# Performance work log

Hardware: AMD Instinct MI355X
Metric: run time of the kernel (lower is better)

Reference implementation:

```python
import jax, jax.numpy as jnp
import numpy as np
from jax import lax

B, C, H, W = 4, 512, 64, 64
C8 = C // 8
OUT = 256
BN_EPS = 1e-5


def setup_inputs() -> dict:
    key = jax.random.key(0)
    ks = jax.random.split(key, 12)
    s = lambda k, shape, fan: jax.random.normal(k, shape, jnp.float32) * (1.0 / np.sqrt(fan))
    return {
        "x": jax.random.normal(ks[0], (B, C, H, W), jnp.float32),
        "wq": s(ks[1], (C8, C), C), "bq": jnp.zeros((C8,), jnp.float32),
        "wk": s(ks[2], (C8, C), C), "bk": jnp.zeros((C8,), jnp.float32),
        "wv": s(ks[3], (C, C), C),  "bv": jnp.zeros((C,), jnp.float32),
        "ca_w1": s(ks[4], (C8, C), C),
        "ca_w2": s(ks[5], (C, C8), C8),
        "conv_w": s(ks[6], (OUT, C, 3, 3), C * 9),
        "bn_gamma": jnp.ones((OUT,), jnp.float32),
        "bn_beta": jnp.zeros((OUT,), jnp.float32),
        "bn_mean": jnp.zeros((OUT,), jnp.float32),
        "bn_var": jnp.ones((OUT,), jnp.float32),
    }


def reference(x, wq, bq, wk, bk, wv, bv, ca_w1, ca_w2, conv_w,
              bn_gamma, bn_beta, bn_mean, bn_var):
    b, c, h, w = x.shape
    n = h * w
    xf = x.reshape(b, c, n)  # [B,C,N]

    # ---- Position attention ----
    q = jnp.einsum('qc,bcn->bnq', wq, xf) + bq            # [B,N,C8]
    k = jnp.einsum('kc,bcn->bkn', wk, xf) + bk[:, None]   # [B,C8,N]
    energy = jnp.einsum('bnq,bqm->bnm', q, k)             # [B,N,N]
    attn = jax.nn.softmax(energy, axis=-1)
    v = jnp.einsum('vc,bcn->bvn', wv, xf) + bv[:, None]   # [B,C,N]
    # torch: bmm(value, attention^T) -> out[b,c,m] = sum_n v[b,c,n]*attn[b,m,n]
    pa = jnp.einsum('bcn,bmn->bcm', v, attn).reshape(b, c, h, w) + x

    # ---- Channel attention (SE-style, avg+max pooled, shared MLP) ----
    avg = jnp.mean(pa, axis=(2, 3))   # [B,C]
    mx = jnp.max(pa, axis=(2, 3))     # [B,C]
    fc = lambda z: jnp.einsum('oc,bc->bo', ca_w2,
                              jax.nn.relu(jnp.einsum('hc,bc->bh', ca_w1, z)))
    scale = jax.nn.sigmoid(fc(avg) + fc(mx))[:, :, None, None]
    ca = scale * pa

    # ---- Conv 3x3 + BN (eval mode) + ReLU ----
    y = lax.conv_general_dilated(ca, conv_w, (1, 1), 'SAME',
                                 dimension_numbers=('NCHW', 'OIHW', 'NCHW'))
    inv = lax.rsqrt(bn_var + BN_EPS)
    y = (y - bn_mean[:, None, None]) * (inv * bn_gamma)[:, None, None] + bn_beta[:, None, None]
    return jax.nn.relu(y)
```

## Files before the change

### kernel.cpp

```cpp
#include <hip/hip_runtime.h>

#define NB 4
#define CIN 512
#define NPIX 4096
#define CQK 64
#define COUT 256
#define PPIX 4356

typedef __bf16 bh16;
typedef _Float16 fh16;
typedef __attribute__((ext_vector_type(8))) __bf16 bf16x8;
typedef __attribute__((ext_vector_type(8))) _Float16 f16x8;
typedef __attribute__((ext_vector_type(16))) float f32x16;

#define AS1 __attribute__((address_space(1)))
#define AS3 __attribute__((address_space(3)))

__device__ __forceinline__ void glds16(const void* g, void* l) {
  __builtin_amdgcn_global_load_lds((const AS1 unsigned int*)g, (AS3 unsigned int*)l, 16, 0, 0);
}

__device__ __forceinline__ float fexp2(float x) {
#if __has_builtin(__builtin_amdgcn_exp2f)
  return __builtin_amdgcn_exp2f(x);
#else
  return __expf(x * 0.6931471805599453f);
#endif
}

__global__ __launch_bounds__(256) void transpose_bf_k(const float* __restrict__ src,
                                                      bh16* __restrict__ dst,
                                                      int rows, int cols) {
  __shared__ float tile[32][33];
  const int b = blockIdx.z;
  const int c0 = blockIdx.x * 32;
  const int r0 = blockIdx.y * 32;
  const float* s = src + (size_t)b * rows * cols;
  bh16* d = dst + (size_t)b * rows * cols;
  const int tx = threadIdx.x, ty = threadIdx.y;
#pragma unroll
  for (int i = 0; i < 32; i += 8)
    tile[ty + i][tx] = s[(size_t)(r0 + ty + i) * cols + (c0 + tx)];
  __syncthreads();
#pragma unroll
  for (int i = 0; i < 32; i += 8)
    d[(size_t)(c0 + ty + i) * rows + (r0 + tx)] = (bh16)tile[tx][ty + i];
}

__global__ __launch_bounds__(256) void wcast_k(const float* __restrict__ wq,
                                               const float* __restrict__ wk,
                                               const float* __restrict__ wv,
                                               const float* __restrict__ bq,
                                               const float* __restrict__ bk,
                                               bh16* __restrict__ Wqk,
                                               bh16* __restrict__ wvb,
                                               float* __restrict__ bias128) {
  const int idx = blockIdx.x * 256 + threadIdx.x;
  if (idx < 65536) {
    Wqk[idx] = (bh16)(idx < 32768 ? wq[idx] : wk[idx - 32768]);
  } else {
    const int j = idx - 65536;
    wvb[j] = (bh16)wv[j];
  }
  if (idx < 128) bias128[idx] = idx < 64 ? bq[idx] : bk[idx - 64];
}

__global__ __launch_bounds__(256) void qk_proj_k(const bh16* __restrict__ xTb,
                                                 const bh16* __restrict__ Wqk,
                                                 const float* __restrict__ bias128,
                                                 bh16* __restrict__ Qb,
                                                 bh16* __restrict__ Kf) {
  const int blk = blockIdx.x;
  const int t = threadIdx.x;
  const int w = t >> 6, l31 = t & 31, hi = (t & 63) >> 5;
  __shared__ __align__(16) bh16 As[2][64 * 64];
  f32x16 acc[2];
#pragma unroll
  for (int nt = 0; nt < 2; nt++)
#pragma unroll
    for (int r = 0; r < 16; r++) acc[nt][r] = 0.0f;

#define QK_STAGE(kc, buf)                                                           \
  {                                                                                 \
    _Pragma("unroll") for (int i = 0; i < 2; i++) {                                 \
      const int s = i * 256 + t;                                                    \
      const int n = s >> 3, slot = s & 7;                                           \
      glds16(xTb + (size_t)(blk * 64 + n) * CIN + (kc) * 64 + (((slot + n) & 7) * 8), \
             &As[buf][(size_t)(i * 256 + w * 64) * 8]);                             \
    }                                                                               \
  }

  QK_STAGE(0, 0);
  __syncthreads();
  for (int kc = 0; kc < 8; kc++) {
    if (kc < 7) QK_STAGE(kc + 1, (kc + 1) & 1);
    const bh16* as = As[kc & 1];
#pragma unroll
    for (int ks = 0; ks < 4; ks++) {
      const bf16x8 bfr = *(const bf16x8*)(Wqk + (size_t)(w * 32 + l31) * CIN + kc * 64 + ks * 16 + hi * 8);
      const int kk = ks * 2 + hi;
#pragma unroll
      for (int nt = 0; nt < 2; nt++) {
        const int n = nt * 32 + l31;
        const bf16x8 a = *(const bf16x8*)&as[(size_t)(n * 8 + ((kk - n) & 7)) * 8];
        acc[nt] = __builtin_amdgcn_mfma_f32_32x32x16_bf16(a, bfr, acc[nt], 0, 0, 0);
      }
    }
    __syncthreads();
  }
#undef QK_STAGE
  const int o = w * 32 + l31;
  const float bo = bias128[o];
  if (w < 2) {
#pragma unroll
    for (int nt = 0; nt < 2; nt++)
#pragma unroll
      for (int r = 0; r < 16; r++) {
        const int nloc = nt * 32 + (r & 3) + 8 * (r >> 2) + 4 * hi;
        Qb[(size_t)(blk * 64 + nloc) * 64 + o] = (bh16)((acc[nt][r] + bo) * 1.44269504088896f);
      }
  } else {
    const int b = blk >> 6, jtile = blk & 63;
    const int k = o - 64, kg = k >> 3, k7 = k & 7;
    bh16* kdst = Kf + (((size_t)(b * 64 + jtile) * 8 + kg) * 64) * 8 + k7;
#pragma unroll
    for (int nt = 0; nt < 2; nt++)
#pragma unroll
      for (int r = 0; r < 16; r++) {
        const int j = nt * 32 + (r & 3) + 8 * (r >> 2) + 4 * hi;
        kdst[(size_t)j * 8] = (bh16)(acc[nt][r] + bo);
      }
  }
}

__global__ __launch_bounds__(256) void v_proj_k(const bh16* __restrict__ xTb,
                                                const bh16* __restrict__ wvb,
                                                const float* __restrict__ bv,
                                                bh16* __restrict__ Vf) {
  const int nblk = blockIdx.x;
  const int cblk = blockIdx.y;
  const int b = blockIdx.z;
  const int t = threadIdx.x;
  const int w = t >> 6, l31 = t & 31, hi = (t & 63) >> 5;
  __shared__ __align__(16) bh16 Bs[2][256 * 64];
  f32x16 acc[2][2];
#pragma unroll
  for (int mt = 0; mt < 2; mt++)
#pragma unroll
    for (int nt = 0; nt < 2; nt++)
#pragma unroll
      for (int r = 0; r < 16; r++) acc[mt][nt][r] = 0.0f;

#define V_STAGE(kc, buf)                                                              \
  {                                                                                   \
    _Pragma("unroll") for (int i = 0; i < 8; i++) {                                   \
      const int s = i * 256 + t;                                                      \
      const int n = s >> 3, slot = s & 7;                                             \
      glds16(xTb + (size_t)(b * NPIX + nblk * 256 + n) * CIN + (kc) * 64 + (((slot + n) & 7) * 8), \
             &Bs[buf][(size_t)(i * 256 + w * 64) * 8]);                               \
    }                                                                                 \
  }

  V_STAGE(0, 0);
  __syncthreads();
  for (int kc = 0; kc < 8; kc++) {
    if (kc < 7) V_STAGE(kc + 1, (kc + 1) & 1);
    const bh16* bs = Bs[kc & 1];
#pragma unroll
    for (int ks = 0; ks < 4; ks++) {
      const int kk = ks * 2 + hi;
      bf16x8 a[2], bfr[2];
#pragma unroll
      for (int mt = 0; mt < 2; mt++)
        a[mt] = *(const bf16x8*)(wvb + (size_t)(cblk * 64 + mt * 32 + l31) * CIN + kc * 64 + ks * 16 + hi * 8);
#pragma unroll
      for (int nt = 0; nt < 2; nt++) {
        const int n = w * 64 + nt * 32 + l31;
        bfr[nt] = *(const bf16x8*)&bs[(size_t)(n * 8 + ((kk - n) & 7)) * 8];
      }
#pragma unroll
      for (int mt = 0; mt < 2; mt++)
#pragma unroll
        for (int nt = 0; nt < 2; nt++)
          acc[mt][nt] = __builtin_amdgcn_mfma_f32_32x32x16_bf16(a[mt], bfr[nt], acc[mt][nt], 0, 0, 0);
    }
    __syncthreads();
  }
#undef V_STAGE
  const int ntile0 = nblk * 4 + w;
#pragma unroll
  for (int mt = 0; mt < 2; mt++)
#pragma unroll
    for (int r = 0; r < 16; r++) {
      const int c = cblk * 64 + mt * 32 + (r & 3) + 8 * (r >> 2) + 4 * hi;
      const float bvc = bv[c];
#pragma unroll
      for (int nt = 0; nt < 2; nt++) {
        const int nl = nt * 32 + l31;
        Vf[(((size_t)(b * 64 + ntile0) * 8 + (nl >> 3)) * 512 + c) * 8 + (nl & 7)] =
            (bh16)(acc[mt][nt][r] + bvc);
      }
    }
}

__global__ __launch_bounds__(256, 2) void attn1p_k(const bh16* __restrict__ Qb,
                                                   const bh16* __restrict__ Kf,
                                                   const bh16* __restrict__ Vf,
                                                   const float* __restrict__ x,
                                                   fh16* __restrict__ pa,
                                                   float* __restrict__ psum,
                                                   float* __restrict__ pmax) {
  const int id = blockIdx.x + 2 * (blockIdx.y + 64 * blockIdx.z);
  const int b = (id & 7) >> 1;
  const int cblk = id & 1;
  const int mblk = (id >> 3) * 64;
  const int t = threadIdx.x;
  const int w = t >> 6, l31 = t & 31, hi = (t >> 5) & 1;
  const int jhalf = w & 1, mhalf = w >> 1;
  __shared__ __align__(16) bh16 Ps[2][8 * 64 * 8];
  __shared__ float lred[4][32];
  __shared__ float linvL[64];

  bf16x8 qf[4];
  {
    const bh16* qrow = Qb + (size_t)(b * NPIX + mblk + mhalf * 32 + l31) * 64;
#pragma unroll
    for (int ks = 0; ks < 4; ks++) qf[ks] = *(const bf16x8*)(qrow + ks * 16 + hi * 8);
  }
  const bh16* kfb = Kf + (size_t)b * (64 * 8 * 64 * 8);
  const bh16* vfb = Vf + (size_t)b * (64 * 8 * 512 * 8);
  const int cbase = cblk * 256 + w * 64;

#define KADDR(tile, ks) (kfb + (((size_t)(tile) * 8 + (ks) * 2 + hi) * 64 + jhalf * 32 + l31) * 8)
#define VADDR(tile, ks, ct) (vfb + (((size_t)(tile) * 8 + (ks) * 2 + hi) * 512 + cbase + (ct) * 32 + l31) * 8)

  f32x16 acc[2][2];
#pragma unroll
  for (int mt = 0; mt < 2; mt++)
#pragma unroll
    for (int ct = 0; ct < 2; ct++)
#pragma unroll
      for (int r = 0; r < 16; r++) acc[mt][ct][r] = 0.0f;
  float4 lsacc;
  lsacc.x = 0.0f; lsacc.y = 0.0f; lsacc.z = 0.0f; lsacc.w = 0.0f;

  bf16x8 kf_nxt[4];
  bf16x8 vf_use[4][2];
  f32x16 s1;
  {
    bf16x8 k0[4];
#pragma unroll
    for (int ks = 0; ks < 4; ks++) {
      k0[ks] = *(const bf16x8*)KADDR(0, ks);
#pragma unroll
      for (int ct = 0; ct < 2; ct++) vf_use[ks][ct] = *(const bf16x8*)VADDR(0, ks, ct);
    }
#pragma unroll
    for (int ks = 0; ks < 4; ks++) kf_nxt[ks] = *(const bf16x8*)KADDR(1, ks);
#pragma unroll
    for (int r = 0; r < 16; r++) s1[r] = 0.0f;
#pragma unroll
    for (int ks = 0; ks < 4; ks++)
      s1 = __builtin_amdgcn_mfma_f32_32x32x16_bf16(k0[ks], qf[ks], s1, 0, 0, 0);
  }

  for (int it = 0; it < 64; it++) {
    f32x16 s1n;
#pragma unroll
    for (int r = 0; r < 16; r++) s1n[r] = 0.0f;
#pragma unroll
    for (int ks = 0; ks < 4; ks++)
      s1n = __builtin_amdgcn_mfma_f32_32x32x16_bf16(kf_nxt[ks], qf[ks], s1n, 0, 0, 0);
    {
      const int kt = (it + 2 < 64) ? it + 2 : 63;
#pragma unroll
      for (int ks = 0; ks < 4; ks++) kf_nxt[ks] = *(const bf16x8*)KADDR(kt, ks);
    }

    const bh16* ps = Ps[(it + 1) & 1];
    bh16* psw = Ps[it & 1];
    if (it) {
#pragma unroll
      for (int ks = 0; ks < 4; ks++) {
        bf16x8 pf0 = *(const bf16x8*)&ps[(size_t)((ks * 2 + hi) * 64 + l31) * 8];
        bf16x8 pf1 = *(const bf16x8*)&ps[(size_t)((ks * 2 + hi) * 64 + 32 + l31) * 8];
        acc[0][0] = __builtin_amdgcn_mfma_f32_32x32x16_bf16(pf0, vf_use[ks][0], acc[0][0], 0, 0, 0);
        acc[0][1] = __builtin_amdgcn_mfma_f32_32x32x16_bf16(pf0, vf_use[ks][1], acc[0][1], 0, 0, 0);
        {
          union { bh16 h[4]; uint2 u2; } pk;
#pragma unroll
          for (int q = 0; q < 4; q++) {
            const float p = fexp2(s1[ks * 4 + q]);
            lsacc[q] += p;
            pk.h[q] = (bh16)p;
          }
          *(uint2*)(void*)&psw[(size_t)((jhalf * 4 + ks) * 64 + mhalf * 32 + l31) * 8 + hi * 4] = pk.u2;
        }
        acc[1][0] = __builtin_amdgcn_mfma_f32_32x32x16_bf16(pf1, vf_use[ks][0], acc[1][0], 0, 0, 0);
        acc[1][1] = __builtin_amdgcn_mfma_f32_32x32x16_bf16(pf1, vf_use[ks][1], acc[1][1], 0, 0, 0);
        vf_use[ks][0] = *(const bf16x8*)VADDR(it, ks, 0);
        vf_use[ks][1] = *(const bf16x8*)VADDR(it, ks, 1);
      }
    } else {
#pragma unroll
      for (int g = 0; g < 4; g++) {
        union { bh16 h[4]; uint2 u2; } pk;
#pragma unroll
        for (int q = 0; q < 4; q++) {
          const float p = fexp2(s1[g * 4 + q]);
          lsacc[q] += p;
          pk.h[q] = (bh16)p;
        }
        *(uint2*)(void*)&psw[(size_t)((jhalf * 4 + g) * 64 + mhalf * 32 + l31) * 8 + hi * 4] = pk.u2;
      }
    }
    __syncthreads();
    s1 = s1n;
  }
  {
    const bh16* ps = Ps[1];
#pragma unroll
    for (int ks = 0; ks < 4; ks++) {
      bf16x8 pf0 = *(const bf16x8*)&ps[(size_t)((ks * 2 + hi) * 64 + l31) * 8];
      bf16x8 pf1 = *(const bf16x8*)&ps[(size_t)((ks * 2 + hi) * 64 + 32 + l31) * 8];
      acc[0][0] = __builtin_amdgcn_mfma_f32_32x32x16_bf16(pf0, vf_use[ks][0], acc[0][0], 0, 0, 0);
      acc[0][1] = __builtin_amdgcn_mfma_f32_32x32x16_bf16(pf0, vf_use[ks][1], acc[0][1], 0, 0, 0);
      acc[1][0] = __builtin_amdgcn_mfma_f32_32x32x16_bf16(pf1, vf_use[ks][0], acc[1][0], 0, 0, 0);
      acc[1][1] = __builtin_amdgcn_mfma_f32_32x32x16_bf16(pf1, vf_use[ks][1], acc[1][1], 0, 0, 0);
    }
  }
#undef KADDR
#undef VADDR

  float lsum = (lsacc.x + lsacc.y) + (lsacc.z + lsacc.w);
  lsum += __shfl_xor(lsum, 32);
  if (hi == 0) lred[w][l31] = lsum;
  __syncthreads();
  if (t < 64) linvL[t] = 1.0f / (lred[(t >> 5) * 2][t & 31] + lred[(t >> 5) * 2 + 1][t & 31]);
  __syncthreads();

  float csum[2] = {0.0f, 0.0f};
  float cmax[2] = {-1e30f, -1e30f};
#pragma unroll
  for (int mt = 0; mt < 2; mt++) {
#pragma unroll
    for (int g = 0; g < 4; g++) {
      const int mloc = mt * 32 + g * 8 + hi * 4;
      const float4 lv = *(const float4*)&linvL[mloc];
#pragma unroll
      for (int ct = 0; ct < 2; ct++) {
        const int c = cbase + ct * 32 + l31;
        const float4 xv = *(const float4*)&x[(size_t)(b * CIN + c) * NPIX + mblk + mloc];
        float r0 = acc[mt][ct][g * 4 + 0] * lv.x + xv.x;
        float r1 = acc[mt][ct][g * 4 + 1] * lv.y + xv.y;
        float r2 = acc[mt][ct][g * 4 + 2] * lv.z + xv.z;
        float r3 = acc[mt][ct][g * 4 + 3] * lv.w + xv.w;
        csum[ct] += (r0 + r1) + (r2 + r3);
        cmax[ct] = fmaxf(cmax[ct], fmaxf(fmaxf(r0, r1), fmaxf(r2, r3)));
        fh16* pd = pa + ((size_t)(b * NPIX) + mblk + mloc) * CIN + c;
        pd[0 * CIN] = (fh16)r0;
        pd[1 * CIN] = (fh16)r1;
        pd[2 * CIN] = (fh16)r2;
        pd[3 * CIN] = (fh16)r3;
      }
    }
  }
#pragma unroll
  for (int ct = 0; ct < 2; ct++) {
    csum[ct] += __shfl_xor(csum[ct], 32);
    cmax[ct] = fmaxf(cmax[ct], __shfl_xor(cmax[ct], 32));
  }
  if (hi == 0) {
    const int mb = mblk >> 6;
#pragma unroll
    for (int ct = 0; ct < 2; ct++) {
      const int c = cbase + ct * 32 + l31;
      psum[((size_t)b * 64 + mb) * CIN + c] = csum[ct];
      pmax[((size_t)b * 64 + mb) * CIN + c] = cmax[ct];
    }
  }
}

__global__ __launch_bounds__(256) void mlp2_k(const float* __restrict__ psum,
                                              const float* __restrict__ pmax,
                                              const float* __restrict__ w1,
                                              const float* __restrict__ w2,
                                              float* __restrict__ scale) {
  const int b = blockIdx.x;
  const int t = threadIdx.x;
  __shared__ float avg_l[CIN], max_l[CIN], hbuf[128];
#pragma unroll
  for (int h = 0; h < 2; h++) {
    const int c = t + h * 256;
    float s = 0.0f, m = -1e30f;
#pragma unroll
    for (int k = 0; k < 64; k++) {
      s += psum[((size_t)b * 64 + k) * CIN + c];
      m = fmaxf(m, pmax[((size_t)b * 64 + k) * CIN + c]);
    }
    avg_l[c] = s * (1.0f / 4096.0f);
    max_l[c] = m;
  }
  __syncthreads();
  if (t < 128) {
    const float* src = (t < 64) ? avg_l : max_l;
    const int o = t & 63;
    float sacc = 0.0f;
    for (int c = 0; c < CIN; c++) sacc += w1[o * CIN + c] * src[c];
    hbuf[t] = fmaxf(sacc, 0.0f);
  }
  __syncthreads();
#pragma unroll
  for (int h = 0; h < 2; h++) {
    const int c = t + h * 256;
    float sacc = 0.0f;
#pragma unroll
    for (int k = 0; k < 64; k++) sacc += w2[c * 64 + k] * (hbuf[k] + hbuf[64 + k]);
    scale[b * CIN + c] = 1.0f / (1.0f + __expf(-sacc));
  }
}

__global__ __launch_bounds__(256) void pack_k(const fh16* __restrict__ pa,
                                              const float* __restrict__ scl,
                                              fh16* __restrict__ pab) {
  const int b = blockIdx.y;
  const int n0 = blockIdx.x * 8;
  const int t = threadIdx.x;
  __shared__ float sc[CIN];
#pragma unroll
  for (int h = 0; h < 2; h++) sc[t + h * 256] = scl[b * CIN + t + h * 256];
  __syncthreads();
  const int c2 = t * 2;
  const float s0 = sc[c2], s1 = sc[c2 + 1];
#pragma unroll
  for (int j = 0; j < 8; j++) {
    const int n = n0 + j;
    const int pp = ((n >> 6) + 1) * 66 + (n & 63) + 1;
    union { fh16 h[2]; unsigned int u; } v, o;
    v.u = *(const unsigned int*)(pa + ((size_t)b * NPIX + n) * CIN + c2);
    o.h[0] = (fh16)((float)v.h[0] * s0);
    o.h[1] = (fh16)((float)v.h[1] * s1);
    *(unsigned int*)(void*)(pab + ((size_t)b * PPIX + pp) * CIN + c2) = o.u;
  }
}

__global__ __launch_bounds__(256) void bzero_k(fh16* __restrict__ pab) {
  const int t = threadIdx.x;
  const int p = blockIdx.x * 4 + (t >> 6);
  const int b = blockIdx.y;
  int pp;
  if (p < 66) pp = p;
  else if (p < 132) pp = 65 * 66 + (p - 66);
  else if (p < 196) pp = (p - 131) * 66;
  else pp = (p - 195) * 66 + 65;
  uint4 z = {0u, 0u, 0u, 0u};
  *(uint4*)(void*)(pab + ((size_t)b * PPIX + pp) * CIN + (t & 63) * 8) = z;
}

__global__ __launch_bounds__(256) void wpack_k(const float* __restrict__ cw,
                                               fh16* __restrict__ wp) {
  const int slot = blockIdx.x * 256 + threadIdx.x;
  const int oblk = slot / 36864;
  const int r1 = slot - oblk * 36864;
  const int chunk = r1 / 1152;
  const int r2 = r1 - chunk * 1152;
  const int tap = r2 >> 7;
  const int r3 = r2 & 127;
  const int h = r3 >> 6;
  const int o = r3 & 63;
  const size_t sbase = (size_t)(oblk * 64 + o) * 4608 + (size_t)(chunk * 16 + h * 8) * 9 + tap;
  union { fh16 h8[8]; uint4 u4; } pk;
#pragma unroll
  for (int i = 0; i < 8; i++) pk.h8[i] = (fh16)cw[sbase + (size_t)i * 9];
  *(uint4*)(void*)(wp + (size_t)slot * 8) = pk.u4;
}

__global__ __launch_bounds__(256) void conv_mfma_k(const fh16* __restrict__ pab,
                                                   const fh16* __restrict__ wp,
                                                   const float* __restrict__ gamma,
                                                   const float* __restrict__ beta,
                                                   const float* __restrict__ mean,
                                                   const float* __restrict__ var,
                                                   float* __restrict__ out) {
  const int y0 = blockIdx.x * 4;
  const int oblk = blockIdx.y;
  const int b = blockIdx.z;
  const int t = threadIdx.x;
  const int w = t >> 6, lane = t & 63, l31 = lane & 31, hi = lane >> 5;
  __shared__ __align__(16) fh16 Xs[2][416 * 16];
  __shared__ __align__(16) fh16 Ws[2][9 * 64 * 16];
  __shared__ float sb[64], bb[64];
  if (t < 64) {
    const int o = oblk * 64 + t;
    const float inv = rsqrtf(var[o] + 1e-5f);
    const float sc = inv * gamma[o];
    sb[t] = sc;
    bb[t] = beta[o] - mean[o] * sc;
  }
  f32x16 o00, o01, o10, o11;
#pragma unroll
  for (int r = 0; r < 16; r++) { o00[r] = 0.0f; o01[r] = 0.0f; o10[r] = 0.0f; o11[r] = 0.0f; }

  const fh16* xbase = pab + ((size_t)b * PPIX + y0 * 66) * CIN + (size_t)(lane & 31) * CIN + (lane >> 5) * 8;
  const fh16* wbase = wp + (size_t)oblk * 32 * 9216 + lane * 8;

#define STAGE(chunk, buf)                                                        \
  {                                                                              \
    const fh16* xs = xbase + (chunk) * 16;                                       \
    for (int i = w; i < 13; i += 4)                                              \
      glds16(xs + (size_t)i * 32 * CIN, &Xs[buf][i * 512]);                      \
    const fh16* wsrc = wbase + (size_t)(chunk) * 9216;                           \
    for (int i = w; i < 18; i += 4)                                              \
      glds16(wsrc + (size_t)i * 512, &Ws[buf][i * 512]);                         \
  }

  STAGE(0, 0);
  __syncthreads();
  for (int chunk = 0; chunk < 32; chunk++) {
    if (chunk < 31) STAGE(chunk + 1, (chunk + 1) & 1);
    const fh16* xs = Xs[chunk & 1];
    const fh16* ws = Ws[chunk & 1];
#pragma unroll
    for (int tap = 0; tap < 9; tap++) {
      const int ky = tap / 3, kx = tap - ky * 3;
      const f16x8 a0 = *(const f16x8*)&ws[tap * 1024 + hi * 512 + l31 * 8];
      const f16x8 a1 = *(const f16x8*)&ws[tap * 1024 + hi * 512 + (32 + l31) * 8];
      const int row0 = (w + ky) * 66 + l31 + kx;
      const int row1 = row0 + 32;
      const f16x8 b0 = *(const f16x8*)&xs[(row0 >> 5) * 512 + hi * 256 + (row0 & 31) * 8];
      const f16x8 b1 = *(const f16x8*)&xs[(row1 >> 5) * 512 + hi * 256 + (row1 & 31) * 8];
      o00 = __builtin_amdgcn_mfma_f32_32x32x16_f16(a0, b0, o00, 0, 0, 0);
      o01 = __builtin_amdgcn_mfma_f32_32x32x16_f16(a0, b1, o01, 0, 0, 0);
      o10 = __builtin_amdgcn_mfma_f32_32x32x16_f16(a1, b0, o10, 0, 0, 0);
      o11 = __builtin_amdgcn_mfma_f32_32x32x16_f16(a1, b1, o11, 0, 0, 0);
    }
    __syncthreads();
  }
#undef STAGE

  const f32x16* accs[2][2] = {{&o00, &o01}, {&o10, &o11}};
#pragma unroll
  for (int mt = 0; mt < 2; mt++) {
#pragma unroll
    for (int nt = 0; nt < 2; nt++) {
      const f32x16& A = *accs[mt][nt];
#pragma unroll
      for (int r = 0; r < 16; r++) {
        const int cl = mt * 32 + (r & 3) + 8 * (r >> 2) + 4 * hi;
        const int pix = nt * 32 + l31;
        const float y = A[r] * sb[cl] + bb[cl];
        out[((size_t)(b * COUT + oblk * 64 + cl)) * NPIX + (y0 + w) * 64 + pix] = fmaxf(y, 0.0f);
      }
    }
  }
}

extern "C" void kernel_launch(void* const* d_in, const int* in_sizes, int n_in,
                              void* d_out, int out_size, void* d_ws, size_t ws_size,
                              hipStream_t stream) {
  (void)in_sizes; (void)n_in; (void)out_size; (void)ws_size;
  const float* x        = (const float*)d_in[0];
  const float* wq       = (const float*)d_in[1];
  const float* bq       = (const float*)d_in[2];
  const float* wk       = (const float*)d_in[3];
  const float* bk       = (const float*)d_in[4];
  const float* wv       = (const float*)d_in[5];
  const float* bv       = (const float*)d_in[6];
  const float* ca_w1    = (const float*)d_in[7];
  const float* ca_w2    = (const float*)d_in[8];
  const float* conv_w   = (const float*)d_in[9];
  const float* bn_gamma = (const float*)d_in[10];
  const float* bn_beta  = (const float*)d_in[11];
  const float* bn_mean  = (const float*)d_in[12];
  const float* bn_var   = (const float*)d_in[13];
  float* out = (float*)d_out;

  float* ws = (float*)d_ws;
  fh16*  pa      = (fh16*)ws;
  float* psum    = ws + 4194304;
  float* pmax    = ws + 4325376;
  bh16*  Vf      = (bh16*)(ws + 8388608);
  fh16*  wpck    = (fh16*)(ws + 8388608);
  bh16*  Qb      = (bh16*)(ws + 12582912);
  bh16*  Kf      = (bh16*)(ws + 13107200);
  bh16*  xTb     = (bh16*)(ws + 13631488);
  fh16*  pab     = (fh16*)(ws + 13631488);
  bh16*  Wqk     = (bh16*)(ws + 17825792);
  bh16*  wvb     = (bh16*)(ws + 17858560);
  float* bias128 = ws + 17989632;
  float* scl     = ws + 18104320;

  wcast_k<<<dim3(1280, 1, 1), 256, 0, stream>>>(wq, wk, wv, bq, bk, Wqk, wvb, bias128);
  transpose_bf_k<<<dim3(NPIX / 32, CIN / 32, NB), dim3(32, 8, 1), 0, stream>>>(x, xTb, CIN, NPIX);
  qk_proj_k<<<dim3(256, 1, 1), 256, 0, stream>>>(xTb, Wqk, bias128, Qb, Kf);
  v_proj_k<<<dim3(16, 8, NB), 256, 0, stream>>>(xTb, wvb, bv, Vf);
  attn1p_k<<<dim3(2, 64, NB), 256, 0, stream>>>(Qb, Kf, Vf, x, pa, psum, pmax);
  bzero_k<<<dim3(65, NB, 1), 256, 0, stream>>>(pab);
  mlp2_k<<<dim3(NB, 1, 1), 256, 0, stream>>>(psum, pmax, ca_w1, ca_w2, scl);
  pack_k<<<dim3(NPIX / 8, NB, 1), 256, 0, stream>>>(pa, scl, pab);
  wpack_k<<<dim3(576, 1, 1), 256, 0, stream>>>(conv_w, wpck);
  conv_mfma_k<<<dim3(16, 4, NB), 256, 0, stream>>>(pab, wpck, bn_gamma, bn_beta,
                                                   bn_mean, bn_var, out);
}
```

Baseline: 320.6 us.

## Widen transpose tiles, relayout attention P buffer, lighten barrier, vectorize MLP loads

The transpose kernel now handles 64x64 tiles with float4 loads and 4-wide bf16 stores, cutting global transaction count. The attention kernel's P staging buffer is laid out as split 4-element halves, which should reduce LDS bank conflicts on the writes. The barrier is replaced with an inline s_waitcnt lgkmcnt(0) plus s_barrier that does not wait on outstanding global loads. The channel-MLP kernel reads its weights with float4 loads. The custom barrier depends on the compiler not reordering memory operations across the inline asm.

```diff
diff --git a/kernel.cpp b/kernel.cpp
--- a/kernel.cpp
+++ b/kernel.cpp
@@ -20,6 +20,10 @@
   __builtin_amdgcn_global_load_lds((const AS1 unsigned int*)g, (AS3 unsigned int*)l, 16, 0, 0);
 }
 
+__device__ __forceinline__ void lbar() {
+  asm volatile("s_waitcnt lgkmcnt(0)\n\ts_barrier" ::: "memory");
+}
+
 __device__ __forceinline__ float fexp2(float x) {
 #if __has_builtin(__builtin_amdgcn_exp2f)
   return __builtin_amdgcn_exp2f(x);
@@ -29,22 +33,36 @@
 }
 
 __global__ __launch_bounds__(256) void transpose_bf_k(const float* __restrict__ src,
-                                                      bh16* __restrict__ dst,
-                                                      int rows, int cols) {
-  __shared__ float tile[32][33];
+                                                      bh16* __restrict__ dst) {
+  __shared__ float tile[64][65];
   const int b = blockIdx.z;
-  const int c0 = blockIdx.x * 32;
-  const int r0 = blockIdx.y * 32;
-  const float* s = src + (size_t)b * rows * cols;
-  bh16* d = dst + (size_t)b * rows * cols;
-  const int tx = threadIdx.x, ty = threadIdx.y;
-#pragma unroll
-  for (int i = 0; i < 32; i += 8)
-    tile[ty + i][tx] = s[(size_t)(r0 + ty + i) * cols + (c0 + tx)];
-  __syncthreads();
-#pragma unroll
-  for (int i = 0; i < 32; i += 8)
-    d[(size_t)(c0 + ty + i) * rows + (r0 + tx)] = (bh16)tile[tx][ty + i];
+  const int n0 = blockIdx.x * 64;
+  const int c0 = blockIdx.y * 64;
+  const float* s = src + (size_t)b * CIN * NPIX;
+  bh16* d = dst + (size_t)b * CIN * NPIX;
+  const int t = threadIdx.x;
+  const int q4 = (t & 15) * 4;
+  const int rr = t >> 4;
+#pragma unroll
+  for (int i = 0; i < 4; i++) {
+    const int c = rr + i * 16;
+    const float4 v = *(const float4*)&s[(size_t)(c0 + c) * NPIX + n0 + q4];
+    tile[q4 + 0][c] = v.x;
+    tile[q4 + 1][c] = v.y;
+    tile[q4 + 2][c] = v.z;
+    tile[q4 + 3][c] = v.w;
+  }
+  __syncthreads();
+#pragma unroll
+  for (int i = 0; i < 4; i++) {
+    const int n = rr + i * 16;
+    union { bh16 h[4]; ushort4 u; } pk;
+    pk.h[0] = (bh16)tile[n][q4 + 0];
+    pk.h[1] = (bh16)tile[n][q4 + 1];
+    pk.h[2] = (bh16)tile[n][q4 + 2];
+    pk.h[3] = (bh16)tile[n][q4 + 3];
+    *(ushort4*)(void*)&d[(size_t)(n0 + n) * CIN + c0 + q4] = pk.u;
+  }
 }
 
 __global__ __launch_bounds__(256) void wcast_k(const float* __restrict__ wq,
@@ -217,7 +235,7 @@
   const int t = threadIdx.x;
   const int w = t >> 6, l31 = t & 31, hi = (t >> 5) & 1;
   const int jhalf = w & 1, mhalf = w >> 1;
-  __shared__ __align__(16) bh16 Ps[2][8 * 64 * 8];
+  __shared__ __align__(16) bh16 Ps[2][8 * 2 * 64 * 4];
   __shared__ float lred[4][32];
   __shared__ float linvL[64];
 
@@ -233,6 +251,11 @@
 
 #define KADDR(tile, ks) (kfb + (((size_t)(tile) * 8 + (ks) * 2 + hi) * 64 + jhalf * 32 + l31) * 8)
 #define VADDR(tile, ks, ct) (vfb + (((size_t)(tile) * 8 + (ks) * 2 + hi) * 512 + cbase + (ct) * 32 + l31) * 8)
+#define PS_RD(f, base)                                                      \
+  {                                                                         \
+    f.u2[0] = *(const uint2*)&ps[(size_t)((base) + l31 * 4)];               \
+    f.u2[1] = *(const uint2*)&ps[(size_t)((base) + 256 + l31 * 4)];         \
+  }
 
   f32x16 acc[2][2];
 #pragma unroll
@@ -282,10 +305,12 @@
     if (it) {
 #pragma unroll
       for (int ks = 0; ks < 4; ks++) {
-        bf16x8 pf0 = *(const bf16x8*)&ps[(size_t)((ks * 2 + hi) * 64 + l31) * 8];
-        bf16x8 pf1 = *(const bf16x8*)&ps[(size_t)((ks * 2 + hi) * 64 + 32 + l31) * 8];
-        acc[0][0] = __builtin_amdgcn_mfma_f32_32x32x16_bf16(pf0, vf_use[ks][0], acc[0][0], 0, 0, 0);
-        acc[0][1] = __builtin_amdgcn_mfma_f32_32x32x16_bf16(pf0, vf_use[ks][1], acc[0][1], 0, 0, 0);
+        const int ks2 = ks * 2 + hi;
+        union { uint2 u2[2]; bf16x8 v; } f0, f1;
+        PS_RD(f0, ks2 * 512);
+        PS_RD(f1, ks2 * 512 + 128);
+        acc[0][0] = __builtin_amdgcn_mfma_f32_32x32x16_bf16(f0.v, vf_use[ks][0], acc[0][0], 0, 0, 0);
+        acc[0][1] = __builtin_amdgcn_mfma_f32_32x32x16_bf16(f0.v, vf_use[ks][1], acc[0][1], 0, 0, 0);
         {
           union { bh16 h[4]; uint2 u2; } pk;
 #pragma unroll
@@ -294,10 +319,10 @@
             lsacc[q] += p;
             pk.h[q] = (bh16)p;
           }
-          *(uint2*)(void*)&psw[(size_t)((jhalf * 4 + ks) * 64 + mhalf * 32 + l31) * 8 + hi * 4] = pk.u2;
+          *(uint2*)(void*)&psw[(size_t)((jhalf * 4 + ks) * 512 + hi * 256 + (mhalf * 32 + l31) * 4)] = pk.u2;
         }
-        acc[1][0] = __builtin_amdgcn_mfma_f32_32x32x16_bf16(pf1, vf_use[ks][0], acc[1][0], 0, 0, 0);
-        acc[1][1] = __builtin_amdgcn_mfma_f32_32x32x16_bf16(pf1, vf_use[ks][1], acc[1][1], 0, 0, 0);
+        acc[1][0] = __builtin_amdgcn_mfma_f32_32x32x16_bf16(f1.v, vf_use[ks][0], acc[1][0], 0, 0, 0);
+        acc[1][1] = __builtin_amdgcn_mfma_f32_32x32x16_bf16(f1.v, vf_use[ks][1], acc[1][1], 0, 0, 0);
         vf_use[ks][0] = *(const bf16x8*)VADDR(it, ks, 0);
         vf_use[ks][1] = *(const bf16x8*)VADDR(it, ks, 1);
       }
@@ -311,26 +336,29 @@
           lsacc[q] += p;
           pk.h[q] = (bh16)p;
         }
-        *(uint2*)(void*)&psw[(size_t)((jhalf * 4 + g) * 64 + mhalf * 32 + l31) * 8 + hi * 4] = pk.u2;
-      }
-    }
-    __syncthreads();
+        *(uint2*)(void*)&psw[(size_t)((jhalf * 4 + g) * 512 + hi * 256 + (mhalf * 32 + l31) * 4)] = pk.u2;
+      }
+    }
+    lbar();
     s1 = s1n;
   }
   {
     const bh16* ps = Ps[1];
 #pragma unroll
     for (int ks = 0; ks < 4; ks++) {
-      bf16x8 pf0 = *(const bf16x8*)&ps[(size_t)((ks * 2 + hi) * 64 + l31) * 8];
-      bf16x8 pf1 = *(const bf16x8*)&ps[(size_t)((ks * 2 + hi) * 64 + 32 + l31) * 8];
-      acc[0][0] = __builtin_amdgcn_mfma_f32_32x32x16_bf16(pf0, vf_use[ks][0], acc[0][0], 0, 0, 0);
-      acc[0][1] = __builtin_amdgcn_mfma_f32_32x32x16_bf16(pf0, vf_use[ks][1], acc[0][1], 0, 0, 0);
-      acc[1][0] = __builtin_amdgcn_mfma_f32_32x32x16_bf16(pf1, vf_use[ks][0], acc[1][0], 0, 0, 0);
-      acc[1][1] = __builtin_amdgcn_mfma_f32_32x32x16_bf16(pf1, vf_use[ks][1], acc[1][1], 0, 0, 0);
+      const int ks2 = ks * 2 + hi;
+      union { uint2 u2[2]; bf16x8 v; } f0, f1;
+      PS_RD(f0, ks2 * 512);
+      PS_RD(f1, ks2 * 512 + 128);
+      acc[0][0] = __builtin_amdgcn_mfma_f32_32x32x16_bf16(f0.v, vf_use[ks][0], acc[0][0], 0, 0, 0);
+      acc[0][1] = __builtin_amdgcn_mfma_f32_32x32x16_bf16(f0.v, vf_use[ks][1], acc[0][1], 0, 0, 0);
+      acc[1][0] = __builtin_amdgcn_mfma_f32_32x32x16_bf16(f1.v, vf_use[ks][0], acc[1][0], 0, 0, 0);
+      acc[1][1] = __builtin_amdgcn_mfma_f32_32x32x16_bf16(f1.v, vf_use[ks][1], acc[1][1], 0, 0, 0);
     }
   }
 #undef KADDR
 #undef VADDR
+#undef PS_RD
 
   float lsum = (lsacc.x + lsacc.y) + (lsacc.z + lsacc.w);
   lsum += __shfl_xor(lsum, 32);
@@ -406,7 +434,10 @@
     const float* src = (t < 64) ? avg_l : max_l;
     const int o = t & 63;
     float sacc = 0.0f;
-    for (int c = 0; c < CIN; c++) sacc += w1[o * CIN + c] * src[c];
+    for (int c = 0; c < CIN; c += 4) {
+      const float4 wv = *(const float4*)&w1[o * CIN + c];
+      sacc += wv.x * src[c] + wv.y * src[c + 1] + wv.z * src[c + 2] + wv.w * src[c + 3];
+    }
     hbuf[t] = fmaxf(sacc, 0.0f);
   }
   __syncthreads();
@@ -415,7 +446,11 @@
     const int c = t + h * 256;
     float sacc = 0.0f;
 #pragma unroll
-    for (int k = 0; k < 64; k++) sacc += w2[c * 64 + k] * (hbuf[k] + hbuf[64 + k]);
+    for (int k = 0; k < 64; k += 4) {
+      const float4 wv = *(const float4*)&w2[c * 64 + k];
+      sacc += wv.x * (hbuf[k] + hbuf[64 + k]) + wv.y * (hbuf[k + 1] + hbuf[64 + k + 1]) +
+              wv.z * (hbuf[k + 2] + hbuf[64 + k + 2]) + wv.w * (hbuf[k + 3] + hbuf[64 + k + 3]);
+    }
     scale[b * CIN + c] = 1.0f / (1.0f + __expf(-sacc));
   }
 }
@@ -591,7 +626,7 @@
   float* scl     = ws + 18104320;
 
   wcast_k<<<dim3(1280, 1, 1), 256, 0, stream>>>(wq, wk, wv, bq, bk, Wqk, wvb, bias128);
-  transpose_bf_k<<<dim3(NPIX / 32, CIN / 32, NB), dim3(32, 8, 1), 0, stream>>>(x, xTb, CIN, NPIX);
+  transpose_bf_k<<<dim3(NPIX / 64, CIN / 64, NB), 256, 0, stream>>>(x, xTb);
   qk_proj_k<<<dim3(256, 1, 1), 256, 0, stream>>>(xTb, Wqk, bias128, Qb, Kf);
   v_proj_k<<<dim3(16, 8, NB), 256, 0, stream>>>(xTb, wvb, bv, Vf);
   attn1p_k<<<dim3(2, 64, NB), 256, 0, stream>>>(Qb, Kf, Vf, x, pa, psum, pmax);
```

Measured after the change: 322.6 us. No clear change (+0.6%).
